# Performance work log

Hardware: AMD Instinct MI355X
Metric: run time of the kernel (lower is better)

## Reference

```python
import jax, jax.numpy as jnp
import numpy as np

# LIF params (from norse LIFParameters in __init__)
DT = 0.001
TAU_SYN_INV = 100.0   # 1/0.01
TAU_MEM_INV = 50.0    # 1/0.02
V_TH = 0.5
V_LEAK = 0.0
V_RESET = 0.0
ALPHA = 100.0         # superspike surrogate slope
# STDP params (additive, hardbound=False)
A_PRE = 0.001
A_POST = 0.001
TAU_PRE_INV = 0.5
TAU_POST_INV = 0.5
ETA_PLUS = 0.01
ETA_MINUS = 0.0001

T_STEPS, BATCH, IN_DIM, HID, N_LBL = 50, 256, 1024, 4096, 10

@jax.custom_vjp
def spike(x):
    return (x >= 0).astype(x.dtype)

def _spike_fwd(x):
    return (x >= 0).astype(x.dtype), x

def _spike_bwd(res, g):
    # norse 'super' (SuperSpike) surrogate gradient
    return (g / (ALPHA * jnp.abs(res) + 1.0) ** 2,)

spike.defvjp(_spike_fwd, _spike_bwd)


def setup_inputs() -> dict:
    key = jax.random.key(0)
    k1, k2, k3, k4 = jax.random.split(key, 4)
    x = (jax.random.uniform(k1, (T_STEPS, BATCH, IN_DIM)) < 0.1).astype(jnp.float32)
    label = jax.random.randint(k2, (BATCH,), 0, N_LBL)
    # positive weights inside the STDP bound [0, 0.3]
    w_in0 = jax.random.uniform(k3, (HID, IN_DIM), dtype=jnp.float32) * 0.3
    w_rec0 = jax.random.uniform(k4, (HID, HID), dtype=jnp.float32) * 0.05
    return {"x": x, "label": label, "w_in0": w_in0, "w_rec0": w_rec0, "num_labels": N_LBL}


def reference(x, label, w_in0, w_rec0, num_labels):
    T, B, I = x.shape
    H = w_in0.shape[0]
    f32 = x.dtype
    # fixed block assignments (init_assignments)
    npd = H // num_labels
    assignments = jnp.clip(jnp.arange(H) // npd, 0, num_labels - 1)
    a = jax.nn.one_hot(assignments, num_labels, dtype=f32)       # (H, L)
    b = jnp.clip(a.sum(axis=0), 1.0, None)                        # (L,)

    def step(carry, pre):
        v, i, z, w_in, w_rec, tp_i, tq_i, tp_r, tq_r, sc = carry
        # --- LIF recurrent cell (norse lif_step semantics) ---
        in_cur = pre @ w_in.T + z @ w_rec.T                       # (B, H)
        v_dec = v + DT * TAU_MEM_INV * ((V_LEAK - v) + i)
        i_dec = i - DT * TAU_SYN_INV * i
        z_new = spike(v_dec - V_TH)
        v_new = (1.0 - z_new) * v_dec + z_new * V_RESET
        i_new = i_dec + in_cur
        # --- STDP on input weights (additive, no hardbound) ---
        tp_i = tp_i + DT * TAU_PRE_INV * (-tp_i + A_PRE * pre)    # (B, I) pre trace
        tq_i = tq_i + DT * TAU_POST_INV * (-tq_i + A_POST * z_new)  # (B, H) post trace
        w_in = (w_in
                + ETA_PLUS * jnp.einsum('bh,bi->hi', z_new, tp_i)
                - ETA_MINUS * jnp.einsum('bh,bi->hi', tq_i, pre))
        # --- STDP on recurrent weights; pre spikes = previous outputs (z) ---
        tp_r = tp_r + DT * TAU_PRE_INV * (-tp_r + A_PRE * z)
        tq_r = tq_r + DT * TAU_POST_INV * (-tq_r + A_POST * z_new)
        w_rec = (w_rec
                 + ETA_PLUS * jnp.einsum('bh,bj->hj', z_new, tp_r)
                 - ETA_MINUS * jnp.einsum('bh,bj->hj', tq_r, z))
        sc = sc + z_new
        return (v_new, i_new, z_new, w_in, w_rec, tp_i, tq_i, tp_r, tq_r, sc), z_new.sum()

    carry0 = (jnp.zeros((B, H), f32), jnp.zeros((B, H), f32), jnp.zeros((B, H), f32),
              w_in0, w_rec0,
              jnp.zeros((B, I), f32), jnp.zeros((B, H), f32),
              jnp.zeros((B, H), f32), jnp.zeros((B, H), f32),
              jnp.zeros((B, H), f32))
    carry, per_t = jax.lax.scan(step, carry0, x)
    _, _, _, w_in_f, w_rec_f, _, _, _, _, sc = carry
    logits = (sc @ a) / (T * b)                                   # (B, L)
    total_spikes = per_t.sum()
    spike_count = jax.ops.segment_sum(sc, label, num_segments=num_labels)  # (L, H)
    label_count = T * jax.ops.segment_sum(jnp.ones((B,), f32), label, num_segments=num_labels)
    return logits, total_spikes, w_in_f, w_rec_f, spike_count, label_count
```

## Files before the change

### kernel.cpp

```cpp
#include <hip/hip_runtime.h>

typedef unsigned short u16;
typedef unsigned char u8;
typedef unsigned int u32;
typedef long i64;
typedef __attribute__((ext_vector_type(4))) float f32x4;
typedef __attribute__((ext_vector_type(4))) int i32x4;

#define TSTEPS 50
#define BB 256
#define II 1024
#define HH 4096
#define LL 10
#define NPLANE ((size_t)BB*HH)
#define HB ((size_t)HH*BB)
#define IB ((size_t)II*BB)
#define TC 10
#define NSLOT 11
#define QSCALE 5.0e6f
#define WSCALE 64.0f

__device__ __forceinline__ u16 f2bf(float f){
  u32 u = __float_as_uint(f);
  u += 0x7fffu + ((u >> 16) & 1u);
  return (u16)(u >> 16);
}
__device__ __forceinline__ float bf2f(u16 u){ return __uint_as_float(((u32)u) << 16); }
__device__ __forceinline__ int wrapslot(int s){ return s >= NSLOT ? s - NSLOT : s; }

__device__ __forceinline__ u8 f2fp8(float v){
  if (v < 0.0009765625f) return 0;
  if (v < 0.015625f) return (u8)__float2int_rn(v * 512.f);
  u32 b = __float_as_uint(v);
  b += 0x7ffffu + ((b >> 20) & 1u);
  int e = (int)((b >> 23) & 255) - 120;
  u32 m = (b >> 20) & 7u;
  return (u8)((e << 3) | m);
}

__device__ __forceinline__ void async_cp16(const void* g, void* l){
  auto gp = (const __attribute__((address_space(1))) void*)(unsigned long long)(g);
  auto lp = (__attribute__((address_space(3))) void*)(unsigned int)(unsigned long long)(l);
  __builtin_amdgcn_global_load_lds(gp, lp, 16, 0, 0);
}

__global__ void __launch_bounds__(256) gemm_fwd(
    const u8* __restrict__ xbt, const u8* __restrict__ wib,
    const u8* __restrict__ zb,  const u8* __restrict__ wrb,
    u16* __restrict__ pbuf)
{
  __shared__ u8 lsA[2][64*64];
  __shared__ u8 lsB[2][64*64];
  const int tid = threadIdx.x, lane = tid & 63, wid = tid >> 6;
  const int wm = wid & 1, wn = wid >> 1;

  int bid = blockIdx.x;
  int xcd = bid & 7;
  int local = bid >> 3;
  int n0 = xcd*512 + (local & 7)*64;
  int rest = local >> 3;
  int z = rest % 5;
  int m0 = (rest / 5)*64;

  const u8* __restrict__ Ab; const u8* __restrict__ Bb;
  int lda, ldb, kbase;
  if (z == 0){ Ab = xbt; lda = II; Bb = wib; ldb = II; kbase = 0; }
  else       { Ab = zb;  lda = HH; Bb = wrb; ldb = HH; kbase = (z-1)*1024; }
  u16* __restrict__ C = pbuf + (size_t)z*NPLANE;

  const int lrow = lane >> 2;
  const int lcb  = (lane & 3) << 4;

  auto STAGE = [&](int buf, int k0){
    int kg = kbase + k0;
    int q = wid;
    int row = q*16 + lrow;
    int cb = lcb ^ (((row >> 1) & 3) << 4);
    async_cp16(Ab + (size_t)(m0 + row)*lda + kg + cb, (char*)lsA[buf] + q*1024);
    async_cp16(Bb + (size_t)(n0 + row)*ldb + kg + cb, (char*)lsB[buf] + q*1024);
  };

  f32x4 acc[2][2];
#pragma unroll
  for (int a=0;a<2;++a)
#pragma unroll
    for (int b=0;b<2;++b) acc[a][b] = f32x4{0.f,0.f,0.f,0.f};

  const int g16 = lane >> 4;
  STAGE(0, 0);
#pragma unroll 1
  for (int kt = 0; kt < 16; ++kt){
    int cur = kt & 1;
    if (kt < 15){
      STAGE(cur ^ 1, (kt+1)*64);
      asm volatile("s_waitcnt vmcnt(2)" ::: "memory");
    } else {
      asm volatile("s_waitcnt vmcnt(0)" ::: "memory");
    }
    __builtin_amdgcn_s_barrier();
#pragma unroll
    for (int kk = 0; kk < 2; ++kk){
      int unit = kk*2 + (g16 >> 1);
      int lo8  = (g16 & 1) << 3;
      i64 af[2], bfr[2];
#pragma unroll
      for (int fm=0; fm<2; ++fm){
        int ra = wm*32 + fm*16 + (lane & 15);
        af[fm] = *(const i64*)((const char*)lsA[cur] + ra*64 +
                               (((unit ^ ((ra >> 1) & 3)) << 4) + lo8));
      }
#pragma unroll
      for (int fn=0; fn<2; ++fn){
        int rb = wn*32 + fn*16 + (lane & 15);
        bfr[fn] = *(const i64*)((const char*)lsB[cur] + rb*64 +
                                (((unit ^ ((rb >> 1) & 3)) << 4) + lo8));
      }
#pragma unroll
      for (int fm=0; fm<2; ++fm)
#pragma unroll
        for (int fn=0; fn<2; ++fn)
          acc[fm][fn] = __builtin_amdgcn_mfma_f32_16x16x32_fp8_fp8(af[fm], bfr[fn], acc[fm][fn], 0, 0, 0);
    }
    __builtin_amdgcn_s_barrier();
  }

#pragma unroll
  for (int fm=0; fm<2; ++fm)
#pragma unroll
    for (int fn=0; fn<2; ++fn)
#pragma unroll
      for (int r=0; r<4; ++r){
        int row = m0 + wm*32 + fm*16 + ((lane >> 4) << 2) + r;
        int col = n0 + wn*32 + fn*16 + (lane & 15);
        C[(size_t)row*HH + col] = f2bf(acc[fm][fn][r]);
      }
}

__global__ void __launch_bounds__(512) gemm_chunk(
    const u8* __restrict__ zRing, const u8* __restrict__ uRing,
    const u8* __restrict__ tpi01s,
    int s0, int first, int lastd,
    float* __restrict__ o_wrec, float* __restrict__ o_win,
    const float* __restrict__ w0rec, const float* __restrict__ w0in,
    float scale)
{
  __shared__ u8 lsA[2][256*64];
  __shared__ u8 lsB[2][256*64];
  const int tid = threadIdx.x, lane = tid & 63, wid = tid >> 6;
  const int xcd = blockIdx.x & 7;
  const int local = blockIdx.x >> 3;
  const int g16 = lane >> 4;
  const int lrow = lane >> 2;
  const int lcb  = (lane & 3) << 4;

  if (local < 32){
    const int wm = wid & 1, wn = wid >> 1;
    int tm = (xcd >> 1)*4 + (local & 3);
    int tn = (xcd & 1)*8 + (local >> 2);
    int m0 = tm*256, n0 = tn*256;

    int offA[2], offB[2], ldso[2];
#pragma unroll
    for (int c=0;c<2;++c){
      int q = c*8 + wid;
      int row = q*16 + lrow;
      int cb = lcb ^ (((row >> 1) & 3) << 4);
      offA[c] = (m0 + row)*BB + cb;
      offB[c] = (n0 + row)*BB + cb;
      ldso[c] = q*1024;
    }

    auto STAGE = [&](int buf, int idx){
      int j  = idx >> 2;
      int k0 = (idx & 3) << 6;
      int sA = wrapslot(s0 + j + 1);
      int sB = wrapslot(s0 + j);
      const u8* __restrict__ Aslab = zRing + (size_t)sA*HB;
      const u8* __restrict__ Bslab = uRing + (size_t)sB*HB;
#pragma unroll
      for (int c=0;c<2;++c){
        async_cp16(Aslab + offA[c] + k0, (char*)lsA[buf] + ldso[c]);
        async_cp16(Bslab + offB[c] + k0, (char*)lsB[buf] + ldso[c]);
      }
    };

    i32x4 acc[8][4];
#pragma unroll
    for (int a=0;a<8;++a)
#pragma unroll
      for (int b=0;b<4;++b) acc[a][b] = i32x4{0,0,0,0};

    STAGE(0, 0);
#pragma unroll 1
    for (int idx = 0; idx < 4*TC; ++idx){
      int cur = idx & 1;
      if (idx < 4*TC-1){
        STAGE(cur ^ 1, idx+1);
        asm volatile("s_waitcnt vmcnt(4)" ::: "memory");
      } else {
        asm volatile("s_waitcnt vmcnt(0)" ::: "memory");
      }
      __builtin_amdgcn_s_barrier();
      __builtin_amdgcn_s_setprio(1);
      i32x4 bfr[4];
#pragma unroll
      for (int fn=0; fn<4; ++fn){
        int rb = wn*64 + fn*16 + (lane & 15);
        bfr[fn] = *(const i32x4*)((const char*)lsB[cur] + rb*64 + ((g16 ^ ((rb >> 1) & 3)) << 4));
      }
#pragma unroll
      for (int fm=0; fm<8; ++fm){
        int ra = wm*128 + fm*16 + (lane & 15);
        i32x4 af = *(const i32x4*)((const char*)lsA[cur] + ra*64 + ((g16 ^ ((ra >> 1) & 3)) << 4));
#pragma unroll
        for (int fn=0; fn<4; ++fn)
          acc[fm][fn] = __builtin_amdgcn_mfma_i32_16x16x64_i8(af, bfr[fn], acc[fm][fn], 0, 0, 0);
      }
      __builtin_amdgcn_s_setprio(0);
      __builtin_amdgcn_s_barrier();
    }

    if (lastd){
#pragma unroll
      for (int fm=0; fm<8; ++fm)
#pragma unroll
        for (int fn=0; fn<4; ++fn)
#pragma unroll
          for (int r=0; r<4; ++r){
            int row = m0 + wm*128 + fm*16 + ((lane >> 4) << 2) + r;
            int col = n0 + wn*64 + fn*16 + (lane & 15);
            size_t cidx = (size_t)row*HH + col;
            o_wrec[cidx] = w0rec[cidx] + scale*((float)acc[fm][fn][r] + o_wrec[cidx]);
          }
    } else if (first){
#pragma unroll
      for (int fm=0; fm<8; ++fm)
#pragma unroll
        for (int fn=0; fn<4; ++fn)
#pragma unroll
          for (int r=0; r<4; ++r){
            int row = m0 + wm*128 + fm*16 + ((lane >> 4) << 2) + r;
            int col = n0 + wn*64 + fn*16 + (lane & 15);
            o_wrec[(size_t)row*HH + col] = (float)acc[fm][fn][r];
          }
    } else {
#pragma unroll
      for (int fm=0; fm<8; ++fm)
#pragma unroll
        for (int fn=0; fn<4; ++fn)
#pragma unroll
          for (int r=0; r<4; ++r){
            int row = m0 + wm*128 + fm*16 + ((lane >> 4) << 2) + r;
            int col = n0 + wn*64 + fn*16 + (lane & 15);
            o_wrec[(size_t)row*HH + col] += (float)acc[fm][fn][r];
          }
    }
  } else {
    const int wm = wid & 1, wn = wid >> 1;
    int l2 = local - 32;
    int tm = (xcd >> 1)*8 + (l2 & 7);
    int tn = (xcd & 1)*4 + (l2 >> 3);
    int m0 = tm*128, n0 = tn*128;

    int offA, offB, ldso;
    {
      int q = wid;
      int row = q*16 + lrow;
      int cb = lcb ^ (((row >> 1) & 3) << 4);
      offA = (m0 + row)*BB + cb;
      offB = (n0 + row)*BB + cb;
      ldso = q*1024;
    }

    auto STAGE = [&](int buf, int idx){
      int j  = idx >> 2;
      int k0 = (idx & 3) << 6;
      int sA = wrapslot(s0 + j + 1);
      const u8* __restrict__ Aslab = zRing + (size_t)sA*HB;
      const u8* __restrict__ Bslab = tpi01s + (size_t)sA*IB;
      async_cp16(Aslab + offA + k0, (char*)lsA[buf] + ldso);
      async_cp16(Bslab + offB + k0, (char*)lsB[buf] + ldso);
    };

    i32x4 acc[4][2];
#pragma unroll
    for (int a=0;a<4;++a)
#pragma unroll
      for (int b=0;b<2;++b) acc[a][b] = i32x4{0,0,0,0};

    STAGE(0, 0);
#pragma unroll 1
    for (int idx = 0; idx < 4*TC; ++idx){
      int cur = idx & 1;
      if (idx < 4*TC-1){
        STAGE(cur ^ 1, idx+1);
        asm volatile("s_waitcnt vmcnt(2)" ::: "memory");
      } else {
        asm volatile("s_waitcnt vmcnt(0)" ::: "memory");
      }
      __builtin_amdgcn_s_barrier();
      __builtin_amdgcn_s_setprio(1);
      i32x4 bfr[2];
#pragma unroll
      for (int fn=0; fn<2; ++fn){
        int rb = wn*32 + fn*16 + (lane & 15);
        bfr[fn] = *(const i32x4*)((const char*)lsB[cur] + rb*64 + ((g16 ^ ((rb >> 1) & 3)) << 4));
      }
#pragma unroll
      for (int fm=0; fm<4; ++fm){
        int ra = wm*64 + fm*16 + (lane & 15);
        i32x4 af = *(const i32x4*)((const char*)lsA[cur] + ra*64 + ((g16 ^ ((ra >> 1) & 3)) << 4));
#pragma unroll
        for (int fn=0; fn<2; ++fn)
          acc[fm][fn] = __builtin_amdgcn_mfma_i32_16x16x64_i8(af, bfr[fn], acc[fm][fn], 0, 0, 0);
      }
      __builtin_amdgcn_s_setprio(0);
      __builtin_amdgcn_s_barrier();
    }

    if (lastd){
#pragma unroll
      for (int fm=0; fm<4; ++fm)
#pragma unroll
        for (int fn=0; fn<2; ++fn)
#pragma unroll
          for (int r=0; r<4; ++r){
            int row = m0 + wm*64 + fm*16 + ((lane >> 4) << 2) + r;
            int col = n0 + wn*32 + fn*16 + (lane & 15);
            size_t cidx = (size_t)row*II + col;
            o_win[cidx] = w0in[cidx] + scale*((float)acc[fm][fn][r] + o_win[cidx]);
          }
    } else if (first){
#pragma unroll
      for (int fm=0; fm<4; ++fm)
#pragma unroll
        for (int fn=0; fn<2; ++fn)
#pragma unroll
          for (int r=0; r<4; ++r){
            int row = m0 + wm*64 + fm*16 + ((lane >> 4) << 2) + r;
            int col = n0 + wn*32 + fn*16 + (lane & 15);
            o_win[(size_t)row*II + col] = (float)acc[fm][fn][r];
          }
    } else {
#pragma unroll
      for (int fm=0; fm<4; ++fm)
#pragma unroll
        for (int fn=0; fn<2; ++fn)
#pragma unroll
          for (int r=0; r<4; ++r){
            int row = m0 + wm*64 + fm*16 + ((lane >> 4) << 2) + r;
            int col = n0 + wn*32 + fn*16 + (lane & 15);
            o_win[(size_t)row*II + col] += (float)acc[fm][fn][r];
          }
    }
  }
}

__device__ __forceinline__ void prep_body(
    const float* __restrict__ x, int t, int i0, int b0, int tid,
    u8* __restrict__ xb_buf, float* __restrict__ tpi,
    u8* __restrict__ tpi01s, int slot,
    u8* ls)
{
  u8 vp[4];
#pragma unroll
  for (int e=0;e<4;++e){
    int f = e*256 + tid;
    int il = f & 63, bl = f >> 6;
    size_t ix = ((size_t)t*BB + b0+bl)*II + i0 + il;
    size_t is = (size_t)(b0+bl)*II + i0 + il;
    float xv = x[ix];
    xb_buf[is] = (xv != 0.f) ? 0x38 : 0;
    float p = tpi[is]; p += 0.0005f*(0.001f*xv - p); tpi[is] = p;
    vp[e] = (u8)__float2int_rn(p * QSCALE);
  }
#pragma unroll
  for (int e=0;e<4;++e){
    int f=e*256+tid; int il=f&63, bl=f>>6;
    ls[il*17+bl] = vp[e];
  }
  __syncthreads();
#pragma unroll
  for (int e=0;e<4;++e){
    int f=e*256+tid; int bl=f&15, il=f>>4;
    size_t oi = (size_t)slot*IB + (size_t)(i0+il)*BB + b0 + bl;
    tpi01s[oi] = ls[il*17+bl];
  }
}

__global__ void __launch_bounds__(256) prep0(
    const float* __restrict__ x, u8* __restrict__ xb_buf,
    float* __restrict__ tpi, u8* __restrict__ tpi01s)
{
  __shared__ u8 ls[64*17];
  int bid = blockIdx.x;
  prep_body(x, 0, (bid & 15)*64, (bid >> 4)*16, threadIdx.x,
            xb_buf, tpi, tpi01s, 1, ls);
}

__global__ void __launch_bounds__(256) step_state(
    const u16* __restrict__ pbuf,
    u16* __restrict__ v, u16* __restrict__ iS, u8* __restrict__ sc,
    u16* __restrict__ u,
    u8* __restrict__ zb, u8* __restrict__ zRing, u8* __restrict__ uRing,
    int slotZ,
    const float* __restrict__ x, int tnext, int do_prep,
    u8* __restrict__ xb_buf, float* __restrict__ tpi,
    u8* __restrict__ tpi01s, int slotP)
{
  __shared__ u8 ls[2][64*17];
  const int tid = threadIdx.x;
  const int bid = blockIdx.x;

  if (bid < 1024){
    const int h0 = (bid & 63) * 64;
    const int b0 = (bid >> 6) * 16;
    u8 vz[4], vu[4];
#pragma unroll
    for (int e=0;e<4;++e){
      int f = e*256 + tid;
      int hl = f & 63, bl = f >> 6;
      size_t idx = (size_t)(b0+bl)*HH + h0 + hl;
      float ic = (bf2f(pbuf[idx]) + bf2f(pbuf[idx + NPLANE]) + bf2f(pbuf[idx + 2*NPLANE])
               +  bf2f(pbuf[idx + 3*NPLANE]) + bf2f(pbuf[idx + 4*NPLANE])) * (1.0f/WSCALE);
      float vv = bf2f(v[idx]), ii = bf2f(iS[idx]);
      float vdec = vv + 0.05f*((0.0f - vv) + ii);
      float idec = ii - 0.1f*ii;
      bool spk = (vdec >= 0.5f);
      float z = spk ? 1.0f : 0.0f;
      v[idx] = spk ? (u16)0 : f2bf(vdec);
      iS[idx] = f2bf(idec + ic);
      float uu = bf2f(u[idx]); uu += 0.0005f*(0.001f*z - uu); u[idx] = f2bf(uu);
      sc[idx] = (u8)(sc[idx] + (spk ? 1 : 0));
      zb[idx] = spk ? 0x38 : 0;
      vz[e] = spk ? 1 : 0;
      vu[e] = (u8)__float2int_rn(uu * QSCALE);
    }
#pragma unroll
    for (int e=0;e<4;++e){
      int f=e*256+tid; int hl=f&63, bl=f>>6; int o = hl*17+bl;
      ls[0][o]=vz[e]; ls[1][o]=vu[e];
    }
    __syncthreads();
#pragma unroll
    for (int e=0;e<4;++e){
      int f=e*256+tid; int bl=f&15, hl=f>>4; int o=hl*17+bl;
      size_t oi = (size_t)slotZ*HB + (size_t)(h0+hl)*BB + b0 + bl;
      zRing[oi]=ls[0][o]; uRing[oi]=ls[1][o];
    }
  } else {
    if (!do_prep) return;
    int r = bid - 1024;
    prep_body(x, tnext, (r & 15)*64, (r >> 4)*16, tid,
              xb_buf, tpi, tpi01s, slotP, ls[0]);
  }
}

__global__ void __launch_bounds__(256) cast_fp8(const f32x4* __restrict__ w0,
                                                u32* __restrict__ wb, long long n4){
  long long i = (long long)blockIdx.x*blockDim.x + threadIdx.x;
  long long stride = (long long)gridDim.x*blockDim.x;
  for (; i < n4; i += stride){
    f32x4 vv = w0[i];
    u32 o = (u32)f2fp8(vv[0]*WSCALE)
          | ((u32)f2fp8(vv[1]*WSCALE) << 8)
          | ((u32)f2fp8(vv[2]*WSCALE) << 16)
          | ((u32)f2fp8(vv[3]*WSCALE) << 24);
    wb[i] = o;
  }
}

__global__ void __launch_bounds__(256) fin_logits(const u8* __restrict__ sc,
                                                  float* __restrict__ logits, float* __restrict__ total){
  __shared__ float bins[LL];
  const int tid = threadIdx.x;
  const int b = blockIdx.x;
  if (tid < LL) bins[tid] = 0.f;
  __syncthreads();
#pragma unroll
  for (int e=0;e<16;++e){
    int h = e*256 + tid;
    float vv = (float)sc[(size_t)b*HH + h];
    int a = h/409; if (a > 9) a = 9;
    atomicAdd(&bins[a], vv);
  }
  __syncthreads();
  if (tid < LL){
    float cnt = (tid==9) ? 415.f : 409.f;
    logits[b*LL + tid] = bins[tid] / (50.f * cnt);
  }
  if (tid == 0){
    float s = 0.f;
    for (int l=0;l<LL;++l) s += bins[l];
    atomicAdd(total, s);
  }
}

__global__ void __launch_bounds__(256) fin_spikecnt(const u8* __restrict__ sc,
                                                    const int* __restrict__ label, float* __restrict__ out){
  int h = blockIdx.x*256 + threadIdx.x;
  int bs = blockIdx.y*32;
  float acc[LL];
#pragma unroll
  for (int j=0;j<LL;++j) acc[j] = 0.f;
  for (int b=bs; b<bs+32; ++b){
    int l = label[b];
    float vv = (float)sc[(size_t)b*HH + h];
#pragma unroll
    for (int j=0;j<LL;++j) acc[j] += (j==l) ? vv : 0.f;
  }
#pragma unroll
  for (int j=0;j<LL;++j)
    if (acc[j] != 0.f) atomicAdd(&out[(size_t)j*HH + h], acc[j]);
}

__global__ void __launch_bounds__(256) fin_labelcnt(const int* __restrict__ label, float* __restrict__ out){
  __shared__ int bins[LL];
  const int tid = threadIdx.x;
  if (tid < LL) bins[tid] = 0;
  __syncthreads();
  atomicAdd(&bins[label[tid]], 1);
  __syncthreads();
  if (tid < LL) out[tid] = 50.f * (float)bins[tid];
}

extern "C" void kernel_launch(void* const* d_in, const int* in_sizes, int n_in,
                              void* d_out, int out_size, void* d_ws, size_t ws_size,
                              hipStream_t stream)
{
  (void)in_sizes; (void)n_in; (void)out_size; (void)ws_size;
  const float* x      = (const float*)d_in[0];
  const int*   label  = (const int*)d_in[1];
  const float* w_in0  = (const float*)d_in[2];
  const float* w_rec0 = (const float*)d_in[3];

  float* out      = (float*)d_out;
  float* o_logits = out;
  float* o_total  = out + 2560;
  float* o_win    = out + 2561;
  float* o_wrec   = o_win + (size_t)HH*II;
  float* o_sc     = o_wrec + (size_t)HH*HH;
  float* o_lc     = o_sc + (size_t)LL*HH;

  char* cur = (char*)d_ws;
  auto alloc = [&](size_t bytes)->char*{ char* p = cur; cur += (bytes + 255) & ~(size_t)255; return p; };
  u8*    wib    = (u8*)   alloc((size_t)HH*II);
  u8*    wrb    = (u8*)   alloc((size_t)HH*HH);
  u16*   v      = (u16*)  alloc(NPLANE*2);
  u16*   iS     = (u16*)  alloc(NPLANE*2);
  u8*    sc     = (u8*)   alloc(NPLANE);
  u16*   u      = (u16*)  alloc(NPLANE*2);
  u16*   pbuf   = (u16*)  alloc(5*NPLANE*2);
  u8*    zb     = (u8*)   alloc(NPLANE);
  u8*    xb_buf = (u8*)   alloc((size_t)BB*II);
  float* tpi    = (float*)alloc((size_t)BB*II*4);
  u8*    zRing  = (u8*)   alloc((size_t)NSLOT*HB);
  u8*    uRing  = (u8*)   alloc((size_t)NSLOT*HB);
  u8*    tpi01s = (u8*)   alloc((size_t)NSLOT*IB);

  hipMemsetAsync(v,     0, NPLANE*2, stream);
  hipMemsetAsync(iS,    0, NPLANE*2, stream);
  hipMemsetAsync(sc,    0, NPLANE, stream);
  hipMemsetAsync(u,     0, NPLANE*2, stream);
  hipMemsetAsync(zb,    0, NPLANE, stream);
  hipMemsetAsync(tpi,   0, (size_t)BB*II*4, stream);
  hipMemsetAsync(zRing, 0, HB, stream);
  hipMemsetAsync(uRing, 0, HB, stream);
  hipMemsetAsync(o_total, 0, 4, stream);
  hipMemsetAsync(o_sc,  0, (size_t)LL*HH*4, stream);

  cast_fp8<<<1024, 256, 0, stream>>>((const f32x4*)w_in0,  (u32*)wib, (long long)HH*II/4);
  cast_fp8<<<2048, 256, 0, stream>>>((const f32x4*)w_rec0, (u32*)wrb, (long long)HH*HH/4);
  prep0<<<256, 256, 0, stream>>>(x, xb_buf, tpi, tpi01s);

  for (int t = 0; t < TSTEPS; ++t){
    gemm_fwd<<<1280, 256, 0, stream>>>(xb_buf, wib, zb, wrb, pbuf);

    step_state<<<1280, 256, 0, stream>>>(
        pbuf, v, iS, sc, u, zb, zRing, uRing, (t+1) % NSLOT,
        x, t+1, (t < TSTEPS-1) ? 1 : 0,
        xb_buf, tpi, tpi01s, (t+2) % NSLOT);

    if ((t+1) % TC == 0){
      int s0 = (t+1-TC) % NSLOT;
      gemm_chunk<<<512, 512, 0, stream>>>(zRing, uRing, tpi01s,
                                          s0, (t+1 == TC) ? 1 : 0,
                                          (t+1 == TSTEPS) ? 1 : 0,
                                          o_wrec, o_win, w_rec0, w_in0,
                                          0.01f/QSCALE);
    }
  }

  fin_logits  <<<BB, 256, 0, stream>>>(sc, o_logits, o_total);
  fin_spikecnt<<<dim3(HH/256, 8), 256, 0, stream>>>(sc, label, o_sc);
  fin_labelcnt<<<1, 256, 0, stream>>>(label, o_lc);
}
```

Before: 1.650 ms.

## Fuse forward GEMM with LIF state update and drop split-K partial buffer

The split-K forward GEMM (5 planes of bf16 partials) and the separate step_state kernel are merged into one kernel. Each block runs the full K=5120 reduction and applies the LIF update in its epilogue, with the next step's input prep running in extra blocks. The z and xb buffers are double-buffered so reads and writes within one launch do not conflict. This removes the 5-plane partial write and re-read and one launch per step, but drops the grid from 1280 to 256 GEMM blocks, each with a 5x longer K loop, which leaves many CUs idle.

```diff
diff --git a/kernel.cpp b/kernel.cpp
--- a/kernel.cpp
+++ b/kernel.cpp
@@ -44,40 +44,82 @@
   __builtin_amdgcn_global_load_lds(gp, lp, 16, 0, 0);
 }
 
-__global__ void __launch_bounds__(256) gemm_fwd(
-    const u8* __restrict__ xbt, const u8* __restrict__ wib,
-    const u8* __restrict__ zb,  const u8* __restrict__ wrb,
-    u16* __restrict__ pbuf)
+__device__ __forceinline__ void prep_body(
+    const float* __restrict__ x, int t, int i0, int b0, int tid,
+    u8* __restrict__ xb_buf, float* __restrict__ tpi,
+    u8* __restrict__ tpi01s, int slot,
+    u8* ls)
+{
+  u8 vp[4];
+#pragma unroll
+  for (int e=0;e<4;++e){
+    int f = e*256 + tid;
+    int il = f & 63, bl = f >> 6;
+    size_t ix = ((size_t)t*BB + b0+bl)*II + i0 + il;
+    size_t is = (size_t)(b0+bl)*II + i0 + il;
+    float xv = x[ix];
+    xb_buf[is] = (xv != 0.f) ? 0x38 : 0;
+    float p = tpi[is]; p += 0.0005f*(0.001f*xv - p); tpi[is] = p;
+    vp[e] = (u8)__float2int_rn(p * QSCALE);
+  }
+#pragma unroll
+  for (int e=0;e<4;++e){
+    int f=e*256+tid; int il=f&63, bl=f>>6;
+    ls[il*17+bl] = vp[e];
+  }
+  __syncthreads();
+#pragma unroll
+  for (int e=0;e<4;++e){
+    int f=e*256+tid; int bl=f&15, il=f>>4;
+    size_t oi = (size_t)slot*IB + (size_t)(i0+il)*BB + b0 + bl;
+    tpi01s[oi] = ls[il*17+bl];
+  }
+}
+
+__global__ void __launch_bounds__(256) fwd_step(
+    const u8* __restrict__ xbR, const u8* __restrict__ wib,
+    const u8* __restrict__ zbR, const u8* __restrict__ wrb,
+    u16* __restrict__ v, u16* __restrict__ iS, u8* __restrict__ sc,
+    u16* __restrict__ u,
+    u8* __restrict__ zbW, u8* __restrict__ zRing, u8* __restrict__ uRing,
+    int slotZ,
+    const float* __restrict__ x, int tnext, int do_prep,
+    u8* __restrict__ xbW, float* __restrict__ tpi,
+    u8* __restrict__ tpi01s, int slotP)
 {
   __shared__ u8 lsA[2][64*64];
   __shared__ u8 lsB[2][64*64];
+  __shared__ u8 tT[2][64*65];
   const int tid = threadIdx.x, lane = tid & 63, wid = tid >> 6;
+  const int bid = blockIdx.x;
+
+  if (bid >= 256){
+    if (!do_prep) return;
+    int r = bid - 256;
+    prep_body(x, tnext, (r & 15)*64, (r >> 4)*16, tid,
+              xbW, tpi, tpi01s, slotP, tT[0]);
+    return;
+  }
+
   const int wm = wid & 1, wn = wid >> 1;
-
-  int bid = blockIdx.x;
   int xcd = bid & 7;
   int local = bid >> 3;
   int n0 = xcd*512 + (local & 7)*64;
-  int rest = local >> 3;
-  int z = rest % 5;
-  int m0 = (rest / 5)*64;
-
-  const u8* __restrict__ Ab; const u8* __restrict__ Bb;
-  int lda, ldb, kbase;
-  if (z == 0){ Ab = xbt; lda = II; Bb = wib; ldb = II; kbase = 0; }
-  else       { Ab = zb;  lda = HH; Bb = wrb; ldb = HH; kbase = (z-1)*1024; }
-  u16* __restrict__ C = pbuf + (size_t)z*NPLANE;
+  int m0 = (local >> 3)*64;
 
   const int lrow = lane >> 2;
   const int lcb  = (lane & 3) << 4;
 
-  auto STAGE = [&](int buf, int k0){
-    int kg = kbase + k0;
+  auto STAGE = [&](int buf, int kt){
+    const u8* __restrict__ A; const u8* __restrict__ B;
+    int lda, k0;
+    if (kt < 16){ A = xbR; B = wib; lda = II; k0 = kt << 6; }
+    else        { A = zbR; B = wrb; lda = HH; k0 = (kt-16) << 6; }
     int q = wid;
     int row = q*16 + lrow;
     int cb = lcb ^ (((row >> 1) & 3) << 4);
-    async_cp16(Ab + (size_t)(m0 + row)*lda + kg + cb, (char*)lsA[buf] + q*1024);
-    async_cp16(Bb + (size_t)(n0 + row)*ldb + kg + cb, (char*)lsB[buf] + q*1024);
+    async_cp16(A + (size_t)(m0 + row)*lda + k0 + cb, (char*)lsA[buf] + q*1024);
+    async_cp16(B + (size_t)(n0 + row)*lda + k0 + cb, (char*)lsB[buf] + q*1024);
   };
 
   f32x4 acc[2][2];
@@ -89,10 +131,10 @@
   const int g16 = lane >> 4;
   STAGE(0, 0);
 #pragma unroll 1
-  for (int kt = 0; kt < 16; ++kt){
+  for (int kt = 0; kt < 80; ++kt){
     int cur = kt & 1;
-    if (kt < 15){
-      STAGE(cur ^ 1, (kt+1)*64);
+    if (kt < 79){
+      STAGE(cur ^ 1, kt+1);
       asm volatile("s_waitcnt vmcnt(2)" ::: "memory");
     } else {
       asm volatile("s_waitcnt vmcnt(0)" ::: "memory");
@@ -130,10 +172,32 @@
     for (int fn=0; fn<2; ++fn)
 #pragma unroll
       for (int r=0; r<4; ++r){
-        int row = m0 + wm*32 + fm*16 + ((lane >> 4) << 2) + r;
-        int col = n0 + wn*32 + fn*16 + (lane & 15);
-        C[(size_t)row*HH + col] = f2bf(acc[fm][fn][r]);
-      }
+        int rloc = wm*32 + fm*16 + (g16 << 2) + r;
+        int cloc = wn*32 + fn*16 + (lane & 15);
+        size_t idx = (size_t)(m0 + rloc)*HH + n0 + cloc;
+        float ic = acc[fm][fn][r] * (1.0f/WSCALE);
+        float vv = bf2f(v[idx]), ii = bf2f(iS[idx]);
+        float vdec = vv + 0.05f*((0.0f - vv) + ii);
+        float idec = ii - 0.1f*ii;
+        bool spk = (vdec >= 0.5f);
+        float z = spk ? 1.0f : 0.0f;
+        v[idx] = spk ? (u16)0 : f2bf(vdec);
+        iS[idx] = f2bf(idec + ic);
+        float uu = bf2f(u[idx]); uu += 0.0005f*(0.001f*z - uu); u[idx] = f2bf(uu);
+        sc[idx] = (u8)(sc[idx] + (spk ? 1 : 0));
+        zbW[idx] = spk ? 0x38 : 0;
+        tT[0][cloc*65 + rloc] = spk ? 1 : 0;
+        tT[1][cloc*65 + rloc] = (u8)__float2int_rn(uu * QSCALE);
+      }
+  __syncthreads();
+#pragma unroll
+  for (int e=0; e<16; ++e){
+    int f = e*256 + tid;
+    int bl = f & 63, hl = f >> 6;
+    size_t oi = (size_t)slotZ*HB + (size_t)(n0 + hl)*BB + m0 + bl;
+    zRing[oi] = tT[0][hl*65 + bl];
+    uRing[oi] = tT[1][hl*65 + bl];
+  }
 }
 
 __global__ void __launch_bounds__(512) gemm_chunk(
@@ -356,38 +420,6 @@
   }
 }
 
-__device__ __forceinline__ void prep_body(
-    const float* __restrict__ x, int t, int i0, int b0, int tid,
-    u8* __restrict__ xb_buf, float* __restrict__ tpi,
-    u8* __restrict__ tpi01s, int slot,
-    u8* ls)
-{
-  u8 vp[4];
-#pragma unroll
-  for (int e=0;e<4;++e){
-    int f = e*256 + tid;
-    int il = f & 63, bl = f >> 6;
-    size_t ix = ((size_t)t*BB + b0+bl)*II + i0 + il;
-    size_t is = (size_t)(b0+bl)*II + i0 + il;
-    float xv = x[ix];
-    xb_buf[is] = (xv != 0.f) ? 0x38 : 0;
-    float p = tpi[is]; p += 0.0005f*(0.001f*xv - p); tpi[is] = p;
-    vp[e] = (u8)__float2int_rn(p * QSCALE);
-  }
-#pragma unroll
-  for (int e=0;e<4;++e){
-    int f=e*256+tid; int il=f&63, bl=f>>6;
-    ls[il*17+bl] = vp[e];
-  }
-  __syncthreads();
-#pragma unroll
-  for (int e=0;e<4;++e){
-    int f=e*256+tid; int bl=f&15, il=f>>4;
-    size_t oi = (size_t)slot*IB + (size_t)(i0+il)*BB + b0 + bl;
-    tpi01s[oi] = ls[il*17+bl];
-  }
-}
-
 __global__ void __launch_bounds__(256) prep0(
     const float* __restrict__ x, u8* __restrict__ xb_buf,
     float* __restrict__ tpi, u8* __restrict__ tpi01s)
@@ -396,64 +428,6 @@
   int bid = blockIdx.x;
   prep_body(x, 0, (bid & 15)*64, (bid >> 4)*16, threadIdx.x,
             xb_buf, tpi, tpi01s, 1, ls);
-}
-
-__global__ void __launch_bounds__(256) step_state(
-    const u16* __restrict__ pbuf,
-    u16* __restrict__ v, u16* __restrict__ iS, u8* __restrict__ sc,
-    u16* __restrict__ u,
-    u8* __restrict__ zb, u8* __restrict__ zRing, u8* __restrict__ uRing,
-    int slotZ,
-    const float* __restrict__ x, int tnext, int do_prep,
-    u8* __restrict__ xb_buf, float* __restrict__ tpi,
-    u8* __restrict__ tpi01s, int slotP)
-{
-  __shared__ u8 ls[2][64*17];
-  const int tid = threadIdx.x;
-  const int bid = blockIdx.x;
-
-  if (bid < 1024){
-    const int h0 = (bid & 63) * 64;
-    const int b0 = (bid >> 6) * 16;
-    u8 vz[4], vu[4];
-#pragma unroll
-    for (int e=0;e<4;++e){
-      int f = e*256 + tid;
-      int hl = f & 63, bl = f >> 6;
-      size_t idx = (size_t)(b0+bl)*HH + h0 + hl;
-      float ic = (bf2f(pbuf[idx]) + bf2f(pbuf[idx + NPLANE]) + bf2f(pbuf[idx + 2*NPLANE])
-               +  bf2f(pbuf[idx + 3*NPLANE]) + bf2f(pbuf[idx + 4*NPLANE])) * (1.0f/WSCALE);
-      float vv = bf2f(v[idx]), ii = bf2f(iS[idx]);
-      float vdec = vv + 0.05f*((0.0f - vv) + ii);
-      float idec = ii - 0.1f*ii;
-      bool spk = (vdec >= 0.5f);
-      float z = spk ? 1.0f : 0.0f;
-      v[idx] = spk ? (u16)0 : f2bf(vdec);
-      iS[idx] = f2bf(idec + ic);
-      float uu = bf2f(u[idx]); uu += 0.0005f*(0.001f*z - uu); u[idx] = f2bf(uu);
-      sc[idx] = (u8)(sc[idx] + (spk ? 1 : 0));
-      zb[idx] = spk ? 0x38 : 0;
-      vz[e] = spk ? 1 : 0;
-      vu[e] = (u8)__float2int_rn(uu * QSCALE);
-    }
-#pragma unroll
-    for (int e=0;e<4;++e){
-      int f=e*256+tid; int hl=f&63, bl=f>>6; int o = hl*17+bl;
-      ls[0][o]=vz[e]; ls[1][o]=vu[e];
-    }
-    __syncthreads();
-#pragma unroll
-    for (int e=0;e<4;++e){
-      int f=e*256+tid; int bl=f&15, hl=f>>4; int o=hl*17+bl;
-      size_t oi = (size_t)slotZ*HB + (size_t)(h0+hl)*BB + b0 + bl;
-      zRing[oi]=ls[0][o]; uRing[oi]=ls[1][o];
-    }
-  } else {
-    if (!do_prep) return;
-    int r = bid - 1024;
-    prep_body(x, tnext, (r & 15)*64, (r >> 4)*16, tid,
-              xb_buf, tpi, tpi01s, slotP, ls[0]);
-  }
 }
 
 __global__ void __launch_bounds__(256) cast_fp8(const f32x4* __restrict__ w0,
@@ -550,19 +524,23 @@
   u16*   iS     = (u16*)  alloc(NPLANE*2);
   u8*    sc     = (u8*)   alloc(NPLANE);
   u16*   u      = (u16*)  alloc(NPLANE*2);
-  u16*   pbuf   = (u16*)  alloc(5*NPLANE*2);
-  u8*    zb     = (u8*)   alloc(NPLANE);
-  u8*    xb_buf = (u8*)   alloc((size_t)BB*II);
+  u8*    zb0    = (u8*)   alloc(NPLANE);
+  u8*    zb1    = (u8*)   alloc(NPLANE);
+  u8*    xb0    = (u8*)   alloc((size_t)BB*II);
+  u8*    xb1    = (u8*)   alloc((size_t)BB*II);
   float* tpi    = (float*)alloc((size_t)BB*II*4);
   u8*    zRing  = (u8*)   alloc((size_t)NSLOT*HB);
   u8*    uRing  = (u8*)   alloc((size_t)NSLOT*HB);
   u8*    tpi01s = (u8*)   alloc((size_t)NSLOT*IB);
+  u8* zb[2] = {zb0, zb1};
+  u8* xb[2] = {xb0, xb1};
 
   hipMemsetAsync(v,     0, NPLANE*2, stream);
   hipMemsetAsync(iS,    0, NPLANE*2, stream);
   hipMemsetAsync(sc,    0, NPLANE, stream);
   hipMemsetAsync(u,     0, NPLANE*2, stream);
-  hipMemsetAsync(zb,    0, NPLANE, stream);
+  hipMemsetAsync(zb0,   0, NPLANE, stream);
+  hipMemsetAsync(zb1,   0, NPLANE, stream);
   hipMemsetAsync(tpi,   0, (size_t)BB*II*4, stream);
   hipMemsetAsync(zRing, 0, HB, stream);
   hipMemsetAsync(uRing, 0, HB, stream);
@@ -571,15 +549,15 @@
 
   cast_fp8<<<1024, 256, 0, stream>>>((const f32x4*)w_in0,  (u32*)wib, (long long)HH*II/4);
   cast_fp8<<<2048, 256, 0, stream>>>((const f32x4*)w_rec0, (u32*)wrb, (long long)HH*HH/4);
-  prep0<<<256, 256, 0, stream>>>(x, xb_buf, tpi, tpi01s);
+  prep0<<<256, 256, 0, stream>>>(x, xb[0], tpi, tpi01s);
 
   for (int t = 0; t < TSTEPS; ++t){
-    gemm_fwd<<<1280, 256, 0, stream>>>(xb_buf, wib, zb, wrb, pbuf);
-
-    step_state<<<1280, 256, 0, stream>>>(
-        pbuf, v, iS, sc, u, zb, zRing, uRing, (t+1) % NSLOT,
+    fwd_step<<<512, 256, 0, stream>>>(
+        xb[t & 1], wib, zb[t & 1], wrb,
+        v, iS, sc, u,
+        zb[(t+1) & 1], zRing, uRing, (t+1) % NSLOT,
         x, t+1, (t < TSTEPS-1) ? 1 : 0,
-        xb_buf, tpi, tpi01s, (t+2) % NSLOT);
+        xb[(t+1) & 1], tpi, tpi01s, (t+2) % NSLOT);
 
     if ((t+1) % TC == 0){
       int s0 = (t+1-TC) % NSLOT;
```

Result: slower. 2.162 ms (+31.0%).
